# Performance work log

Hardware: AMD Instinct MI355X
Metric: run time of the kernel (lower is better)

Reference implementation:

```python
import jax, jax.numpy as jnp
import numpy as np

EPS = 1e-5
K = 20


def knn_idx(x, k):
    # x: (B, C, N) -> idx: (B, N, k) of nearest neighbors (self included)
    sq = jnp.sum(x * x, axis=1)  # (B, N)
    # pd[b,n,m] = -||x_n - x_m||^2
    pd = 2.0 * jnp.einsum('bcn,bcm->bnm', x, x) - sq[:, :, None] - sq[:, None, :]
    return jax.lax.top_k(pd, k)[1]


def graph_feature(x, k):
    # x: (B, C, N) -> (B, N, k, 2C) = concat(center, neighbor - center)
    idx = knn_idx(x, k)
    xt = jnp.transpose(x, (0, 2, 1))  # (B, N, C)
    nbr = jax.vmap(lambda t, i: t[i])(xt, idx)  # (B, N, k, C)
    ctr = jnp.broadcast_to(xt[:, :, None, :], nbr.shape)
    return jnp.concatenate([ctr, nbr - ctr], axis=-1)


def conv_bn_lrelu2d(feat, w, g, b):
    # 1x1 Conv2d (bias=False) + BatchNorm2d (training stats) + LeakyReLU(0.2)
    y = jnp.einsum('bnkc,oc->bonk', feat, w)  # (B, O, N, k)
    m = jnp.mean(y, axis=(0, 2, 3), keepdims=True)
    v = jnp.var(y, axis=(0, 2, 3), keepdims=True)
    y = (y - m) / jnp.sqrt(v + EPS) * g[None, :, None, None] + b[None, :, None, None]
    return jax.nn.leaky_relu(y, 0.2)


def reference(x, w1, g1, b1, w2, g2, b2, w3, g3, b3, w4, g4, b4, w5, g5, b5):
    x1 = jnp.max(conv_bn_lrelu2d(graph_feature(x, K), w1, g1, b1), axis=-1)   # (B, 64, N)
    x2 = jnp.max(conv_bn_lrelu2d(graph_feature(x1, K), w2, g2, b2), axis=-1)  # (B, 64, N)
    x3 = jnp.max(conv_bn_lrelu2d(graph_feature(x2, K), w3, g3, b3), axis=-1)  # (B, 128, N)
    x4 = jnp.max(conv_bn_lrelu2d(graph_feature(x3, K), w4, g4, b4), axis=-1)  # (B, 256, N)
    xc = jnp.concatenate([x1, x2, x3, x4], axis=1)  # (B, 512, N)
    y = jnp.einsum('bcn,oc->bon', xc, w5)  # (B, 1024, N)
    m = jnp.mean(y, axis=(0, 2), keepdims=True)
    v = jnp.var(y, axis=(0, 2), keepdims=True)
    y = (y - m) / jnp.sqrt(v + EPS) * g5[None, :, None] + b5[None, :, None]
    y = jax.nn.leaky_relu(y, 0.2)
    return jnp.max(y, axis=-1)  # (B, 1024)


def setup_inputs() -> dict:
    key = jax.random.key(0)
    ks = jax.random.split(key, 6)
    B, N = 8, 2048
    s = 0.02
    return {
        'x': jax.random.normal(ks[0], (B, 3, N), dtype=jnp.float32),
        'w1': jax.random.normal(ks[1], (64, 6), dtype=jnp.float32) * s,
        'g1': jnp.ones((64,), jnp.float32), 'b1': jnp.zeros((64,), jnp.float32),
        'w2': jax.random.normal(ks[2], (64, 128), dtype=jnp.float32) * s,
        'g2': jnp.ones((64,), jnp.float32), 'b2': jnp.zeros((64,), jnp.float32),
        'w3': jax.random.normal(ks[3], (128, 128), dtype=jnp.float32) * s,
        'g3': jnp.ones((128,), jnp.float32), 'b3': jnp.zeros((128,), jnp.float32),
        'w4': jax.random.normal(ks[4], (256, 256), dtype=jnp.float32) * s,
        'g4': jnp.ones((256,), jnp.float32), 'b4': jnp.zeros((256,), jnp.float32),
        'w5': jax.random.normal(ks[5], (1024, 512), dtype=jnp.float32) * s,
        'g5': jnp.ones((1024,), jnp.float32), 'b5': jnp.zeros((1024,), jnp.float32),
    }
```

## Files before the change

### kernel.cpp

```cpp
#include <hip/hip_runtime.h>
#include <hip/hip_bf16.h>
#include <math.h>

#define BB 8
#define NN 2048
#define KK 20
#define XCCH 512
#define NSLOT 64
#define LEPS 1e-5f
#define NEGINF -3.4e38f

typedef __attribute__((ext_vector_type(8))) short s8v;
typedef __attribute__((ext_vector_type(8))) _Float16 h8v;
typedef __attribute__((ext_vector_type(4))) float f32x4;

__device__ __forceinline__ float lrelu(float x){ return x >= 0.f ? x : 0.2f*x; }

__global__ __launch_bounds__(256) void k_transpose(const float* __restrict__ x, float* __restrict__ xt){
  int i = blockIdx.x*256 + threadIdx.x;
  if (i >= BB*NN) return;
  int b = i >> 11, n = i & (NN-1);
  float4 v;
  v.x = x[(b*3+0)*NN + n];
  v.y = x[(b*3+1)*NN + n];
  v.z = x[(b*3+2)*NN + n];
  v.w = 0.f;
  reinterpret_cast<float4*>(xt)[i] = v;
}

__global__ __launch_bounds__(256) void k_cvtw(const float* __restrict__ W, __hip_bfloat16* __restrict__ Wb,
                                              int Cs, int coff, int Ccnt, int Cpad, int total){
  int i = blockIdx.x*256 + threadIdx.x;
  if (i >= total) return;
  int o = i / Cpad, c = i - o*Cpad;
  Wb[i] = (c < Ccnt) ? __float2bfloat16(W[(size_t)o*Cs + coff + c]) : __float2bfloat16(0.f);
}

__global__ __launch_bounds__(256) void k_split(const float* __restrict__ P, int stride, int Ci, int Cpad,
    _Float16* __restrict__ Ph, _Float16* __restrict__ Pl){
  int i = blockIdx.x*256 + threadIdx.x;
  if (i >= BB*NN*Cpad) return;
  int p = i / Cpad, c = i - p*Cpad;
  float v = (c < Ci) ? P[(size_t)p*stride + c] : 0.f;
  _Float16 h = (_Float16)v;
  float r = v - (float)h;
  Ph[i] = h;
  Pl[i] = (_Float16)r;
}

__global__ __launch_bounds__(256) void k_sqs(const _Float16* __restrict__ Ph,
    const _Float16* __restrict__ Pl, int Cpad, float* __restrict__ sq){
  int i = blockIdx.x*256 + threadIdx.x;
  if (i >= BB*NN) return;
  const _Float16* ph = Ph + (size_t)i*Cpad;
  const _Float16* pl = Pl + (size_t)i*Cpad;
  float s = 0.f;
  for (int c = 0; c < Cpad; ++c){
    float v = (float)ph[c] + (float)pl[c];
    s += v*v;
  }
  sq[i] = s;
}

__global__ __launch_bounds__(256) void k_distm(
    const _Float16* __restrict__ Ph, const _Float16* __restrict__ Pl,
    int Cpad, int nchunk, const float* __restrict__ sq, float* __restrict__ pd)
{
  __shared__ _Float16 Ah[128*40];
  __shared__ _Float16 Al[128*40];
  __shared__ _Float16 Bh[128*40];
  __shared__ _Float16 Bl[128*40];
  int t = threadIdx.x;
  int w = t >> 6, lane = t & 63, m = lane & 15, quad = lane >> 4;
  int b = blockIdx.z;
  int n0 = blockIdx.y * 128, m0 = blockIdx.x * 128;
  const _Float16* PhB = Ph + (size_t)b*NN*Cpad;
  const _Float16* PlB = Pl + (size_t)b*NN*Cpad;
  f32x4 acc[2][8];
  #pragma unroll
  for (int s=0;s<2;s++)
    #pragma unroll
    for (int j=0;j<8;j++){ f32x4 z = {0.f,0.f,0.f,0.f}; acc[s][j] = z; }
  int r = t >> 1;
  int sg0 = t & 1;
  for (int ch=0; ch<nchunk; ++ch){
    int c0 = ch*32;
    #pragma unroll
    for (int k=0;k<2;k++){
      int seg = sg0 + 2*k;
      int go = c0 + seg*8;
      size_t an = (size_t)(n0+r)*Cpad + go;
      size_t bm = (size_t)(m0+r)*Cpad + go;
      *(h8v*)&Ah[r*40 + seg*8] = *(const h8v*)&PhB[an];
      *(h8v*)&Al[r*40 + seg*8] = *(const h8v*)&PlB[an];
      *(h8v*)&Bh[r*40 + seg*8] = *(const h8v*)&PhB[bm];
      *(h8v*)&Bl[r*40 + seg*8] = *(const h8v*)&PlB[bm];
    }
    __syncthreads();
    h8v ah0 = *(const h8v*)&Ah[(w*32 + m)*40 + quad*8];
    h8v al0 = *(const h8v*)&Al[(w*32 + m)*40 + quad*8];
    h8v ah1 = *(const h8v*)&Ah[(w*32 + 16 + m)*40 + quad*8];
    h8v al1 = *(const h8v*)&Al[(w*32 + 16 + m)*40 + quad*8];
    #pragma unroll
    for (int j=0;j<8;j++){
      h8v bh = *(const h8v*)&Bh[(j*16 + m)*40 + quad*8];
      h8v bl = *(const h8v*)&Bl[(j*16 + m)*40 + quad*8];
      acc[0][j] = __builtin_amdgcn_mfma_f32_16x16x32_f16(ah0, bh, acc[0][j], 0, 0, 0);
      acc[0][j] = __builtin_amdgcn_mfma_f32_16x16x32_f16(ah0, bl, acc[0][j], 0, 0, 0);
      acc[0][j] = __builtin_amdgcn_mfma_f32_16x16x32_f16(al0, bh, acc[0][j], 0, 0, 0);
      acc[0][j] = __builtin_amdgcn_mfma_f32_16x16x32_f16(al0, bl, acc[0][j], 0, 0, 0);
      acc[1][j] = __builtin_amdgcn_mfma_f32_16x16x32_f16(ah1, bh, acc[1][j], 0, 0, 0);
      acc[1][j] = __builtin_amdgcn_mfma_f32_16x16x32_f16(ah1, bl, acc[1][j], 0, 0, 0);
      acc[1][j] = __builtin_amdgcn_mfma_f32_16x16x32_f16(al1, bh, acc[1][j], 0, 0, 0);
      acc[1][j] = __builtin_amdgcn_mfma_f32_16x16x32_f16(al1, bl, acc[1][j], 0, 0, 0);
    }
    __syncthreads();
  }
  float sqm_[8];
  #pragma unroll
  for (int j=0;j<8;j++) sqm_[j] = sq[b*NN + m0 + j*16 + m];
  #pragma unroll
  for (int s=0;s<2;s++){
    int rbase = w*32 + s*16 + quad*4;
    #pragma unroll
    for (int rg=0; rg<4; rg++){
      float sqn = sq[b*NN + n0 + rbase + rg];
      size_t rowoff = ((size_t)b*NN + n0 + rbase + rg)*NN + m0 + m;
      #pragma unroll
      for (int j=0;j<8;j++){
        pd[rowoff + j*16] = 2.f*acc[s][j][rg] - sqn - sqm_[j];
      }
    }
  }
}

#define TK_REP32(F) F(0)F(1)F(2)F(3)F(4)F(5)F(6)F(7)F(8)F(9)F(10)F(11)F(12)F(13)F(14)F(15) \
                    F(16)F(17)F(18)F(19)F(20)F(21)F(22)F(23)F(24)F(25)F(26)F(27)F(28)F(29)F(30)F(31)
#define TK_SCAN(u) { bool c1 = r##u > p1; bool c2 = r##u > p2; \
                     p2 = c1 ? p1 : (c2 ? r##u : p2); i1 = c1 ? u : i1; p1 = c1 ? r##u : p1; }
#define TK_CLR(u)  r##u = (i1 == u) ? NEGINF : r##u;

__global__ __launch_bounds__(256) void k_topk(const float* __restrict__ pd, int* __restrict__ idxo){
  int t = threadIdx.x;
  int l = t & 63;
  int row = blockIdx.x*4 + (t >> 6);
  const float4* rp = (const float4*)(pd + (size_t)row*NN);
  float4 q0 = rp[0*64+l], q1 = rp[1*64+l], q2 = rp[2*64+l], q3 = rp[3*64+l];
  float4 q4 = rp[4*64+l], q5 = rp[5*64+l], q6 = rp[6*64+l], q7 = rp[7*64+l];
  float r0 =q0.x, r1 =q0.y, r2 =q0.z, r3 =q0.w, r4 =q1.x, r5 =q1.y, r6 =q1.z, r7 =q1.w;
  float r8 =q2.x, r9 =q2.y, r10=q2.z, r11=q2.w, r12=q3.x, r13=q3.y, r14=q3.z, r15=q3.w;
  float r16=q4.x, r17=q4.y, r18=q4.z, r19=q4.w, r20=q5.x, r21=q5.y, r22=q5.z, r23=q5.w;
  float r24=q6.x, r25=q6.y, r26=q6.z, r27=q6.w, r28=q7.x, r29=q7.y, r30=q7.z, r31=q7.w;
  float p1 = NEGINF, p2 = NEGINF; int i1 = 0;
  TK_REP32(TK_SCAN)
  int* orow = idxo + (size_t)row*KK;
  int got = 0;
  while (got < KK){
    float M2 = p2;
    #pragma unroll
    for (int off=1; off<64; off<<=1) M2 = fmaxf(M2, __shfl_xor(M2, off));
    bool ex = (p1 >= M2);
    unsigned long long ball = __ballot(ex);
    int cnt = __popcll(ball);
    int take = KK - got;
    if (cnt <= take){
      if (ex){
        int pos = got + __popcll(ball & ((1ull << l) - 1ull));
        orow[pos] = ((i1 >> 2) << 8) | (l << 2) | (i1 & 3);
      }
      got += cnt;
      if (ex && got < KK){
        TK_REP32(TK_CLR)
        p1 = NEGINF; p2 = NEGINF; i1 = 0;
        TK_REP32(TK_SCAN)
      }
    } else {
      for (int tt = 0; tt < take; ++tt){
        float wv = p1;
        #pragma unroll
        for (int off=1; off<64; off<<=1) wv = fmaxf(wv, __shfl_xor(wv, off));
        int gi = (p1 == wv) ? (((i1 >> 2) << 8) | (l << 2) | (i1 & 3)) : 0x7FFFFFFF;
        int cand = gi;
        #pragma unroll
        for (int off=1; off<64; off<<=1){
          int oc = __shfl_xor(cand, off);
          cand = oc < cand ? oc : cand;
        }
        if (gi == cand){
          orow[got + tt] = cand;
          p1 = NEGINF;
        }
      }
      got = KK;
    }
  }
}

__global__ __launch_bounds__(256) void k_wprep(const float* __restrict__ W, int Ci, int Oi,
                                               float* __restrict__ W2){
  int i = blockIdx.x*256 + threadIdx.x;
  if (i >= 2*Oi*Ci) return;
  int r = i / Ci, c = i - r*Ci;
  if (r < Oi){
    W2[i] = W[(size_t)r*2*Ci + Ci + c];
  } else {
    int o = r - Oi;
    W2[i] = W[(size_t)o*2*Ci + c] - W[(size_t)o*2*Ci + Ci + c];
  }
}

__global__ __launch_bounds__(256) void k_gemmud(const float* __restrict__ P, int stride, int Ci,
    const float* __restrict__ W2, int ostr, float* __restrict__ udb){
  __shared__ float Pt[16*68];
  __shared__ float Wt[16*68];
  int t = threadIdx.x, ty = t >> 4, tx = t & 15;
  int p0 = blockIdx.x*64, o0 = blockIdx.y*64;
  float acc[4][4];
  #pragma unroll
  for (int i=0;i<4;i++)
    #pragma unroll
    for (int j=0;j<4;j++) acc[i][j]=0.f;
  for (int c0 = 0; c0 < Ci; c0 += 16){
    #pragma unroll
    for (int q=0;q<4;q++){
      int e = t + 256*q;
      int r = e >> 4, cc = e & 15;
      int c = c0 + cc;
      bool ok = (c < Ci);
      Pt[cc*68 + r] = ok ? P[(size_t)(p0+r)*stride + c] : 0.f;
      Wt[cc*68 + r] = ok ? W2[(size_t)(o0+r)*Ci + c] : 0.f;
    }
    __syncthreads();
    #pragma unroll
    for (int j=0;j<16;j++){
      float4 av  = *(const float4*)&Pt[j*68 + ty*4];
      float4 bv4 = *(const float4*)&Wt[j*68 + tx*4];
      float a[4]  = {av.x, av.y, av.z, av.w};
      float bv[4] = {bv4.x, bv4.y, bv4.z, bv4.w};
      #pragma unroll
      for (int i=0;i<4;i++)
        #pragma unroll
        for (int jj=0;jj<4;jj++) acc[i][jj] += a[i]*bv[jj];
    }
    __syncthreads();
  }
  #pragma unroll
  for (int i=0;i<4;i++){
    *(float4*)&udb[(size_t)(p0+ty*4+i)*ostr + o0 + tx*4] =
      make_float4(acc[i][0], acc[i][1], acc[i][2], acc[i][3]);
  }
}

__global__ __launch_bounds__(256) void k_edge(const float* __restrict__ udb, int ostr, int Oi,
    const int* __restrict__ idxg,
    float* __restrict__ ymax, float* __restrict__ ymin,
    float* __restrict__ chsum, float* __restrict__ chsq){
  __shared__ int lidx[16*KK];
  __shared__ float reds[2][4][64];
  int t = threadIdx.x, w = t >> 6, lane = t & 63;
  int n0 = blockIdx.x*16;
  int b  = n0 >> 11;
  int o0 = blockIdx.y*64;
  for (int q=t; q<16*KK; q+=256) lidx[q] = idxg[(size_t)n0*KK + q];
  __syncthreads();
  int o = o0 + lane;
  float ws_s = 0.f, ws_q = 0.f;
  #pragma unroll
  for (int p=0;p<4;p++){
    int pl = w*4 + p;
    int n = n0 + pl;
    float mx = -3.4e38f, mn = 3.4e38f, s = 0.f, s2 = 0.f;
    #pragma unroll
    for (int k=0;k<KK;k++){
      int nb = lidx[pl*KK + k];
      float u = udb[(size_t)((b<<11) + nb)*ostr + o];
      mx = fmaxf(mx, u); mn = fminf(mn, u);
      s += u; s2 += u*u;
    }
    float Dv = udb[(size_t)n*ostr + Oi + o];
    size_t base = (size_t)n*256 + o;
    ymax[base] = mx + Dv;
    ymin[base] = mn + Dv;
    ws_s += s + (float)KK*Dv;
    ws_q += s2 + 2.f*Dv*s + (float)KK*Dv*Dv;
  }
  reds[0][w][lane] = ws_s;
  reds[1][w][lane] = ws_q;
  __syncthreads();
  if (w == 0){
    float s = reds[0][0][lane] + reds[0][1][lane] + reds[0][2][lane] + reds[0][3][lane];
    float q = reds[1][0][lane] + reds[1][1][lane] + reds[1][2][lane] + reds[1][3][lane];
    int slot = blockIdx.x & (NSLOT-1);
    atomicAdd(&chsum[slot*256 + o], s);
    atomicAdd(&chsq [slot*256 + o], q);
  }
}

__global__ __launch_bounds__(256) void k_bnstats(const float* __restrict__ chsum, const float* __restrict__ chsq,
    const float* __restrict__ g, const float* __restrict__ bet,
    float* __restrict__ scl, float* __restrict__ shf, int Oi){
  int o = threadIdx.x;
  if (o >= Oi) return;
  float s=0.f, s2=0.f;
  for (int u=0;u<NSLOT;u++){ s += chsum[u*256+o]; s2 += chsq[u*256+o]; }
  float cnt = (float)(BB*NN*KK);
  float mean = s/cnt;
  float var = s2/cnt - mean*mean;
  float sc = g[o] / sqrtf(var + LEPS);
  scl[o] = sc;
  shf[o] = bet[o] - mean*sc;
}

__global__ __launch_bounds__(256) void k_apply(const float* __restrict__ ymax, const float* __restrict__ ymin,
    const float* __restrict__ scl, const float* __restrict__ shf,
    float* __restrict__ xc, __hip_bfloat16* __restrict__ xcb, int off, int Oi){
  int i = blockIdx.x*256 + threadIdx.x;
  if (i >= BB*NN*Oi) return;
  int o = i & (Oi-1);
  size_t p = (size_t)((unsigned)i / (unsigned)Oi);
  float sc = scl[o];
  float v = (sc >= 0.f) ? ymax[p*256+o] : ymin[p*256+o];
  float r = lrelu(v*sc + shf[o]);
  xc [p*XCCH + off + o] = r;
  xcb[p*XCCH + off + o] = __float2bfloat16(r);
}

__global__ __launch_bounds__(256) void k_conv5m(const __hip_bfloat16* __restrict__ xcb,
    const __hip_bfloat16* __restrict__ w5b,
    float* __restrict__ pmax, float* __restrict__ pmin,
    float* __restrict__ psum, float* __restrict__ psq)
{
  __shared__ __align__(16) char smem[20480];
  __hip_bfloat16* As = (__hip_bfloat16*)smem;
  __hip_bfloat16* Bs = (__hip_bfloat16*)(smem + 10240);
  float* red = (float*)smem;
  int t = threadIdx.x, w = t >> 6, lane = t & 63, m = lane & 15, quad = lane >> 4;
  int nbk = blockIdx.x;
  int b = blockIdx.z;
  int o0 = blockIdx.y * 128;
  int n0 = nbk * 128;
  const __hip_bfloat16* Abase = xcb + (size_t)(b*NN + n0)*XCCH;
  const __hip_bfloat16* Bbase = w5b + (size_t)o0*XCCH;
  f32x4 acc[2][8];
  #pragma unroll
  for (int s=0;s<2;s++)
    #pragma unroll
    for (int j=0;j<8;j++){ f32x4 z = {0.f,0.f,0.f,0.f}; acc[s][j] = z; }
  int r = t >> 1;
  int sg0 = t & 1;
  for (int ch=0; ch<16; ++ch){
    int c0 = ch*32;
    #pragma unroll
    for (int k=0;k<2;k++){
      int seg = sg0 + 2*k;
      int go = c0 + seg*8;
      *(s8v*)&As[r*40 + seg*8] = *(const s8v*)&Abase[(size_t)r*XCCH + go];
      *(s8v*)&Bs[r*40 + seg*8] = *(const s8v*)&Bbase[(size_t)r*XCCH + go];
    }
    __syncthreads();
    s8v a0 = *(const s8v*)&As[(w*32 + m)*40 + quad*8];
    s8v a1 = *(const s8v*)&As[(w*32 + 16 + m)*40 + quad*8];
    #pragma unroll
    for (int j=0;j<8;j++){
      s8v bf = *(const s8v*)&Bs[(j*16 + m)*40 + quad*8];
      acc[0][j] = __builtin_amdgcn_mfma_f32_16x16x32_bf16(a0, bf, acc[0][j], 0, 0, 0);
      acc[1][j] = __builtin_amdgcn_mfma_f32_16x16x32_bf16(a1, bf, acc[1][j], 0, 0, 0);
    }
    __syncthreads();
  }
  float mx[8], mn[8], sm[8], sq[8];
  #pragma unroll
  for (int j=0;j<8;j++){
    mx[j] = -3.4e38f; mn[j] = 3.4e38f; sm[j] = 0.f; sq[j] = 0.f;
    #pragma unroll
    for (int s=0;s<2;s++){
      f32x4 a = acc[s][j];
      #pragma unroll
      for (int rg=0; rg<4; rg++){
        float v = a[rg];
        mx[j] = fmaxf(mx[j], v); mn[j] = fminf(mn[j], v);
        sm[j] += v; sq[j] += v*v;
      }
    }
  }
  #pragma unroll
  for (int j=0;j<8;j++){
    #pragma unroll
    for (int off=16; off<=32; off<<=1){
      mx[j] = fmaxf(mx[j], __shfl_xor(mx[j], off));
      mn[j] = fminf(mn[j], __shfl_xor(mn[j], off));
      sm[j] += __shfl_xor(sm[j], off);
      sq[j] += __shfl_xor(sq[j], off);
    }
  }
  if (quad == 0){
    #pragma unroll
    for (int j=0;j<8;j++){
      int c = j*16 + m;
      red[(0*4 + w)*128 + c] = mx[j];
      red[(1*4 + w)*128 + c] = mn[j];
      red[(2*4 + w)*128 + c] = sm[j];
      red[(3*4 + w)*128 + c] = sq[j];
    }
  }
  __syncthreads();
  if (t < 128){
    int c = t;
    float MX = red[(0*4+0)*128+c], MN = red[(1*4+0)*128+c];
    float S  = red[(2*4+0)*128+c], Q  = red[(3*4+0)*128+c];
    #pragma unroll
    for (int u=1;u<4;u++){
      MX = fmaxf(MX, red[(0*4+u)*128+c]);
      MN = fminf(MN, red[(1*4+u)*128+c]);
      S += red[(2*4+u)*128+c];
      Q += red[(3*4+u)*128+c];
    }
    size_t ii = ((size_t)b*1024 + o0 + c)*16 + nbk;
    pmax[ii] = MX; pmin[ii] = MN; psum[ii] = S; psq[ii] = Q;
  }
}

__global__ __launch_bounds__(256) void k_stats5(const float* __restrict__ psum, const float* __restrict__ psq,
    const float* __restrict__ g5, const float* __restrict__ b5,
    float* __restrict__ sc5, float* __restrict__ sh5){
  int o = blockIdx.x*256 + threadIdx.x;
  float s=0.f, s2=0.f;
  for (int b=0;b<BB;b++){
    const float* ps = &psum[((size_t)b*1024 + o)*16];
    const float* pq = &psq [((size_t)b*1024 + o)*16];
    #pragma unroll
    for (int u=0;u<16;u++){ s += ps[u]; s2 += pq[u]; }
  }
  float cnt = (float)(BB*NN);
  float mean = s/cnt;
  float var = s2/cnt - mean*mean;
  float sc = g5[o] / sqrtf(var + LEPS);
  sc5[o] = sc;
  sh5[o] = b5[o] - mean*sc;
}

__global__ __launch_bounds__(256) void k_apply5(const float* __restrict__ pmax, const float* __restrict__ pmin,
    const float* __restrict__ sc5, const float* __restrict__ sh5, float* __restrict__ out){
  int i = blockIdx.x*256 + threadIdx.x;
  int o = i & 1023;
  float sc = sc5[o];
  float v;
  if (sc >= 0.f){
    const float* p = &pmax[(size_t)i*16];
    v = p[0];
    #pragma unroll
    for (int u=1;u<16;u++) v = fmaxf(v, p[u]);
  } else {
    const float* p = &pmin[(size_t)i*16];
    v = p[0];
    #pragma unroll
    for (int u=1;u<16;u++) v = fminf(v, p[u]);
  }
  out[i] = lrelu(v*sc + sh5[o]);
}

extern "C" void kernel_launch(void* const* d_in, const int* in_sizes, int n_in,
                              void* d_out, int out_size, void* d_ws, size_t ws_size,
                              hipStream_t stream){
  const float* x  = (const float*)d_in[0];
  const float* w1 = (const float*)d_in[1];
  const float* g1 = (const float*)d_in[2];
  const float* b1 = (const float*)d_in[3];
  const float* w2 = (const float*)d_in[4];
  const float* g2 = (const float*)d_in[5];
  const float* b2 = (const float*)d_in[6];
  const float* w3 = (const float*)d_in[7];
  const float* g3 = (const float*)d_in[8];
  const float* b3 = (const float*)d_in[9];
  const float* w4 = (const float*)d_in[10];
  const float* g4 = (const float*)d_in[11];
  const float* b4 = (const float*)d_in[12];
  const float* w5 = (const float*)d_in[13];
  const float* g5 = (const float*)d_in[14];
  const float* b5 = (const float*)d_in[15];
  float* out = (float*)d_out;
  float* ws = (float*)d_ws;

  const size_t F_PD   = 0;
  const size_t F_XT0  = F_PD   + (size_t)BB*NN*NN;
  const size_t F_XC   = F_XT0  + (size_t)BB*NN*4;
  const size_t F_CHS  = F_XC   + (size_t)BB*NN*XCCH;
  const size_t F_CHQ  = F_CHS  + (size_t)NSLOT*256;
  const size_t F_SCL  = F_CHQ  + (size_t)NSLOT*256;
  const size_t F_SHF  = F_SCL  + 256;
  const size_t F_SQ   = F_SHF  + 256;
  const size_t F_IDX  = F_SQ   + (size_t)BB*NN;
  const size_t F_PMAX = F_IDX  + (size_t)BB*NN*KK;
  const size_t F_PMIN = F_PMAX + (size_t)BB*1024*8;
  const size_t F_PSUM = F_PMIN + (size_t)BB*1024*8;
  const size_t F_PSQ  = F_PSUM + (size_t)BB*1024*8;
  const size_t F_SC5  = F_PSQ  + (size_t)BB*1024*8;
  const size_t F_SH5  = F_SC5  + 1024;
  const size_t F_XCB  = F_SH5  + 1024;
  const size_t F_WB   = F_XCB  + (size_t)BB*NN*XCCH/2;
  const size_t F_PH   = F_WB   + 278528;
  const size_t F_PL   = F_PH   + 1048576;

  float* pd    = ws + F_PD;
  float* udb   = pd;
  float* w2buf = pd + (size_t)12*1024*1024;
  float* ymax  = pd + (size_t)16*1024*1024;
  float* ymin  = pd + (size_t)21*1024*1024;
  float* pmax  = pd;
  float* pmin  = pd + (size_t)(1<<20);
  float* psum  = pd + (size_t)(2<<20);
  float* psq   = pd + (size_t)(3<<20);
  float* xt0   = ws + F_XT0;
  float* xc    = ws + F_XC;
  float* chsum = ws + F_CHS;
  float* chsq  = ws + F_CHQ;
  float* scl   = ws + F_SCL;
  float* shf   = ws + F_SHF;
  float* sqb   = ws + F_SQ;
  int*   idxb  = (int*)(ws + F_IDX);
  float* sc5   = ws + F_SC5;
  float* sh5   = ws + F_SH5;
  __hip_bfloat16* xcb = (__hip_bfloat16*)(ws + F_XCB);
  __hip_bfloat16* wb  = (__hip_bfloat16*)(ws + F_WB);
  __hip_bfloat16* w5b = wb + 32768;
  _Float16* Ph  = (_Float16*)(ws + F_PH);
  _Float16* Pl  = (_Float16*)(ws + F_PL);

  (void)in_sizes; (void)n_in; (void)out_size; (void)ws_size;

  k_transpose<<<64, 256, 0, stream>>>(x, xt0);
  k_cvtw<<<(524288+255)/256, 256, 0, stream>>>(w5, w5b, 512, 0, 512, 512, 524288);

  struct LayerP { const float* P; int stride; int Ci; int CiD; int Cpad;
                  const float* W; const float* g; const float* b; int Oi; int off; };
  LayerP L[4] = {
    { xt0,    4,   3,   4,   32,  w1, g1, b1,  64, 0   },
    { xc,     512, 64,  64,  64,  w2, g2, b2,  64, 64  },
    { xc+64,  512, 64,  64,  64,  w3, g3, b3, 128, 128 },
    { xc+128, 512, 128, 128, 128, w4, g4, b4, 256, 256 },
  };

  for (int l=0; l<4; ++l){
    int Cpad = L[l].Cpad, nchunk = Cpad/32;
    int Oi = L[l].Oi, Ci = L[l].Ci;
    int ostr = 2*Oi;
    k_split<<<(BB*NN*Cpad+255)/256, 256, 0, stream>>>(L[l].P, L[l].stride, L[l].CiD, Cpad, Ph, Pl);
    k_sqs<<<64, 256, 0, stream>>>(Ph, Pl, Cpad, sqb);
    k_distm<<<dim3(16,16,8), 256, 0, stream>>>(Ph, Pl, Cpad, nchunk, sqb, pd);
    k_topk<<<BB*NN/4, 256, 0, stream>>>(pd, idxb);
    hipMemsetAsync(chsum, 0, (size_t)NSLOT*256*2*sizeof(float), stream);
    k_wprep<<<(2*Oi*Ci+255)/256, 256, 0, stream>>>(L[l].W, Ci, Oi, w2buf);
    k_gemmud<<<dim3(BB*NN/64, ostr/64), 256, 0, stream>>>(L[l].P, L[l].stride, Ci, w2buf, ostr, udb);
    k_edge<<<dim3(BB*NN/16, Oi/64), 256, 0, stream>>>(udb, ostr, Oi, idxb, ymax, ymin, chsum, chsq);
    k_bnstats<<<1, 256, 0, stream>>>(chsum, chsq, L[l].g, L[l].b, scl, shf, Oi);
    k_apply<<<(BB*NN*Oi + 255)/256, 256, 0, stream>>>(ymax, ymin, scl, shf, xc, xcb, L[l].off, Oi);
  }

  k_conv5m<<<dim3(16, 8, BB), 256, 0, stream>>>(xcb, w5b, pmax, pmin, psum, psq);
  k_stats5<<<4, 256, 0, stream>>>(psum, psq, g5, b5, sc5, sh5);
  k_apply5<<<(BB*1024)/256, 256, 0, stream>>>(pmax, pmin, sc5, sh5, out);
}
```

Before: 682.2 us.

## Exploit distance-matrix symmetry and keep top-3 per lane in kNN selection

The pairwise distance kernel now launches only the upper-triangular 128x128 tiles (136 per batch) and writes each off-diagonal tile twice, once directly and once transposed, which roughly halves the MFMA work. The transposed store uses float4 writes along columns, giving a more scattered write pattern. Separately, the top-k selection keeps the three best candidates per lane plus a removed-bitmask, so a lane only rescans its 32 registers after two of its entries are consumed. This cuts per-round rescans at the cost of extra register pressure and a more complex selection path.

```diff
diff --git a/kernel.cpp b/kernel.cpp
--- a/kernel.cpp
+++ b/kernel.cpp
@@ -73,7 +73,12 @@
   int t = threadIdx.x;
   int w = t >> 6, lane = t & 63, m = lane & 15, quad = lane >> 4;
   int b = blockIdx.z;
-  int n0 = blockIdx.y * 128, m0 = blockIdx.x * 128;
+  int i = blockIdx.x;
+  int by = (int)((sqrtf(8.f*(float)i + 1.f) - 1.f) * 0.5f);
+  while ((by+1)*(by+2)/2 <= i) by++;
+  while (by*(by+1)/2 > i) by--;
+  int bx = i - by*(by+1)/2;
+  int n0 = by * 128, m0 = bx * 128;
   const _Float16* PhB = Ph + (size_t)b*NN*Cpad;
   const _Float16* PlB = Pl + (size_t)b*NN*Cpad;
   f32x4 acc[2][8];
@@ -119,16 +124,35 @@
   float sqm_[8];
   #pragma unroll
   for (int j=0;j<8;j++) sqm_[j] = sq[b*NN + m0 + j*16 + m];
+  float sqn_[2][4];
+  #pragma unroll
+  for (int s=0;s<2;s++)
+    #pragma unroll
+    for (int rg=0; rg<4; rg++)
+      sqn_[s][rg] = sq[b*NN + n0 + w*32 + s*16 + quad*4 + rg];
   #pragma unroll
   for (int s=0;s<2;s++){
-    int rbase = w*32 + s*16 + quad*4;
     #pragma unroll
     for (int rg=0; rg<4; rg++){
-      float sqn = sq[b*NN + n0 + rbase + rg];
-      size_t rowoff = ((size_t)b*NN + n0 + rbase + rg)*NN + m0 + m;
+      size_t rowoff = ((size_t)b*NN + n0 + w*32 + s*16 + quad*4 + rg)*NN + m0 + m;
       #pragma unroll
       for (int j=0;j<8;j++){
-        pd[rowoff + j*16] = 2.f*acc[s][j][rg] - sqn - sqm_[j];
+        pd[rowoff + j*16] = 2.f*acc[s][j][rg] - sqn_[s][rg] - sqm_[j];
+      }
+    }
+  }
+  if (bx != by){
+    #pragma unroll
+    for (int s=0;s<2;s++){
+      #pragma unroll
+      for (int j=0;j<8;j++){
+        size_t moff = ((size_t)b*NN + m0 + j*16 + m)*NN + n0 + w*32 + s*16 + quad*4;
+        float4 v;
+        v.x = 2.f*acc[s][j][0] - sqm_[j] - sqn_[s][0];
+        v.y = 2.f*acc[s][j][1] - sqm_[j] - sqn_[s][1];
+        v.z = 2.f*acc[s][j][2] - sqm_[j] - sqn_[s][2];
+        v.w = 2.f*acc[s][j][3] - sqm_[j] - sqn_[s][3];
+        *(float4*)&pd[moff] = v;
       }
     }
   }
@@ -136,9 +160,19 @@
 
 #define TK_REP32(F) F(0)F(1)F(2)F(3)F(4)F(5)F(6)F(7)F(8)F(9)F(10)F(11)F(12)F(13)F(14)F(15) \
                     F(16)F(17)F(18)F(19)F(20)F(21)F(22)F(23)F(24)F(25)F(26)F(27)F(28)F(29)F(30)F(31)
-#define TK_SCAN(u) { bool c1 = r##u > p1; bool c2 = r##u > p2; \
-                     p2 = c1 ? p1 : (c2 ? r##u : p2); i1 = c1 ? u : i1; p1 = c1 ? r##u : p1; }
-#define TK_CLR(u)  r##u = (i1 == u) ? NEGINF : r##u;
+#define TK3_SCAN(u) { bool c1 = r##u > p1; bool c2 = r##u > p2; bool c3 = r##u > p3; \
+    p3 = c2 ? p2 : (c3 ? r##u : p3); \
+    i2 = c1 ? i1 : (c2 ? u : i2); \
+    p2 = c1 ? p1 : (c2 ? r##u : p2); \
+    i1 = c1 ? u : i1; \
+    p1 = c1 ? r##u : p1; }
+#define TK3_RSCAN(u) { float vv = ((rem >> u) & 1u) ? NEGINF : r##u; \
+    bool c1 = vv > p1; bool c2 = vv > p2; bool c3 = vv > p3; \
+    p3 = c2 ? p2 : (c3 ? vv : p3); \
+    i2 = c1 ? i1 : (c2 ? u : i2); \
+    p2 = c1 ? p1 : (c2 ? vv : p2); \
+    i1 = c1 ? u : i1; \
+    p1 = c1 ? vv : p1; }
 
 __global__ __launch_bounds__(256) void k_topk(const float* __restrict__ pd, int* __restrict__ idxo){
   int t = threadIdx.x;
@@ -151,8 +185,10 @@
   float r8 =q2.x, r9 =q2.y, r10=q2.z, r11=q2.w, r12=q3.x, r13=q3.y, r14=q3.z, r15=q3.w;
   float r16=q4.x, r17=q4.y, r18=q4.z, r19=q4.w, r20=q5.x, r21=q5.y, r22=q5.z, r23=q5.w;
   float r24=q6.x, r25=q6.y, r26=q6.z, r27=q6.w, r28=q7.x, r29=q7.y, r30=q7.z, r31=q7.w;
-  float p1 = NEGINF, p2 = NEGINF; int i1 = 0;
-  TK_REP32(TK_SCAN)
+  float p1 = NEGINF, p2 = NEGINF, p3 = NEGINF;
+  int i1 = 0, i2 = 0, nv = 3;
+  unsigned rem = 0u;
+  TK_REP32(TK3_SCAN)
   int* orow = idxo + (size_t)row*KK;
   int got = 0;
   while (got < KK){
@@ -167,12 +203,14 @@
       if (ex){
         int pos = got + __popcll(ball & ((1ull << l) - 1ull));
         orow[pos] = ((i1 >> 2) << 8) | (l << 2) | (i1 & 3);
+        rem |= 1u << i1;
+        p1 = p2; i1 = i2; p2 = p3; nv--;
       }
       got += cnt;
-      if (ex && got < KK){
-        TK_REP32(TK_CLR)
-        p1 = NEGINF; p2 = NEGINF; i1 = 0;
-        TK_REP32(TK_SCAN)
+      if (got < KK && nv < 2){
+        p1 = NEGINF; p2 = NEGINF; p3 = NEGINF; i1 = 0; i2 = 0;
+        TK_REP32(TK3_RSCAN)
+        nv = 3;
       }
     } else {
       for (int tt = 0; tt < take; ++tt){
@@ -546,7 +584,7 @@
     int ostr = 2*Oi;
     k_split<<<(BB*NN*Cpad+255)/256, 256, 0, stream>>>(L[l].P, L[l].stride, L[l].CiD, Cpad, Ph, Pl);
     k_sqs<<<64, 256, 0, stream>>>(Ph, Pl, Cpad, sqb);
-    k_distm<<<dim3(16,16,8), 256, 0, stream>>>(Ph, Pl, Cpad, nchunk, sqb, pd);
+    k_distm<<<dim3(136,1,8), 256, 0, stream>>>(Ph, Pl, Cpad, nchunk, sqb, pd);
     k_topk<<<BB*NN/4, 256, 0, stream>>>(pd, idxb);
     hipMemsetAsync(chsum, 0, (size_t)NSLOT*256*2*sizeof(float), stream);
     k_wprep<<<(2*Oi*Ci+255)/256, 256, 0, stream>>>(L[l].W, Ci, Oi, w2buf);
```

Result: no change. 676.4 us (-0.9%).
